# Kernel tuning notes

Measured on AMD Instinct MI355X. Metric: run time of the kernel, lower is better.

Reference implementation:

```python
import jax, jax.numpy as jnp
import numpy as np

N = 100000
E = 1600000
IN_C, HID, OUT_C = 3, 64, 1


def setup_inputs() -> dict:
    key = jax.random.key(0)
    ks = jax.random.split(key, 12)
    x = jax.random.normal(ks[0], (N, IN_C), dtype=jnp.float32)
    edge_index = jax.random.randint(ks[1], (2, E), 0, N, dtype=jnp.int64)

    def glorot(k, shape):
        lim = np.sqrt(6.0 / (shape[0] + shape[1]))
        return jax.random.uniform(k, shape, jnp.float32, -lim, lim)

    return {
        "x": x,
        "edge_index": edge_index,
        "W1": glorot(ks[2], (IN_C, HID)), "b1": jnp.zeros((HID,), jnp.float32),
        "W2": glorot(ks[3], (HID, HID)), "b2": jnp.zeros((HID,), jnp.float32),
        "W3": glorot(ks[4], (HID, HID)), "b3": jnp.zeros((HID,), jnp.float32),
        "Wm1": glorot(ks[5], (HID, HID)), "bm1": jnp.zeros((HID,), jnp.float32),
        "Wm2": glorot(ks[6], (HID, OUT_C)), "bm2": jnp.zeros((OUT_C,), jnp.float32),
    }


def gcn_conv(x, src, dst, W, b):
    """PyG GCNConv: symmetric normalization with self-loops, linear, scatter-add, bias."""
    n = x.shape[0]
    loop = jnp.arange(n, dtype=src.dtype)
    s = jnp.concatenate([src, loop])
    d = jnp.concatenate([dst, loop])
    h = x @ W  # (N, out)
    deg = jax.ops.segment_sum(jnp.ones(s.shape[0], dtype=h.dtype), d, num_segments=n)
    dinv = jnp.where(deg > 0, 1.0 / jnp.sqrt(jnp.where(deg > 0, deg, 1.0)), 0.0)
    norm = dinv[s] * dinv[d]  # (E+N,)
    out = jax.ops.segment_sum(h[s] * norm[:, None], d, num_segments=n)
    return out + b


def reference(x, edge_index, W1, b1, W2, b2, W3, b3, Wm1, bm1, Wm2, bm2):
    src, dst = edge_index[0], edge_index[1]
    # 3 GCN layers with ReLU (dropout inactive in eval mode)
    h = jax.nn.relu(gcn_conv(x, src, dst, W1, b1))
    h = jax.nn.relu(gcn_conv(h, src, dst, W2, b2))
    h = jax.nn.relu(gcn_conv(h, src, dst, W3, b3))
    # MLP head + sigmoid
    h = jax.nn.relu(h @ Wm1 + bm1)
    out = jax.nn.sigmoid(h @ Wm2 + bm2)  # (N, 1)
    return out
```

## Files before the change

### kernel.cpp

```cpp
#include <hip/hip_runtime.h>
#include <hip/hip_fp16.h>
#include <math.h>

#define N_NODES 100000
#define N_EDGES 1600000
#define EP (N_EDGES + N_NODES)
#define HID 64
#define NCHUNK 250
#define CE (N_EDGES / NCHUNK)
#define NBUCK 782
#define CAP 2816
#define NTILE (N_NODES / 16)
#define NPN 4

typedef _Float16 half8_t __attribute__((ext_vector_type(8)));
typedef _Float16 half4_t __attribute__((ext_vector_type(4)));
typedef float f32x4_t __attribute__((ext_vector_type(4)));
typedef unsigned long long u64;


__device__ __forceinline__ float fp8_to_f32_1(unsigned b) {
    unsigned s = b >> 7, e = (b >> 3) & 15, m = b & 7;
    float mag = (e == 0) ? (float)m * 0.001953125f
                         : __uint_as_float(((e + 120u) << 23) | (m << 20));
    return s ? -mag : mag;
}

__device__ __forceinline__ unsigned f32_to_fp8_1(float f) {
    unsigned sb = (__float_as_uint(f) >> 31) << 7;
    float a = fabsf(f);
    if (a > 448.f) a = 448.f;
    if (a < 0.001953125f * 0.5f) return sb;
    if (a < 0.015625f) {
        int q = (int)(a * 512.f + 0.5f);
        if (q > 7) return sb | (1u << 3);
        return sb | (unsigned)q;
    }
    unsigned bits = __float_as_uint(a) + (1u << 19);
    int e = (int)((bits >> 23) & 255) - 127;
    unsigned m = (bits >> 20) & 7;
    int ee = e + 7;
    if (ee > 15) { ee = 15; m = 6; }
    return sb | ((unsigned)ee << 3) | m;
}

__device__ __forceinline__ void addp8(float4& a, unsigned w, bool pred) {
    if (pred) {
#if __has_builtin(__builtin_amdgcn_cvt_pk_f32_fp8)
        auto lo = __builtin_amdgcn_cvt_pk_f32_fp8((int)w, false);
        auto hi = __builtin_amdgcn_cvt_pk_f32_fp8((int)w, true);
        a.x += lo[0]; a.y += lo[1]; a.z += hi[0]; a.w += hi[1];
#else
        a.x += fp8_to_f32_1(w & 255);
        a.y += fp8_to_f32_1((w >> 8) & 255);
        a.z += fp8_to_f32_1((w >> 16) & 255);
        a.w += fp8_to_f32_1(w >> 24);
#endif
    }
}

__device__ __forceinline__ unsigned pack_fp8x4(float a, float b, float c, float d) {
#if __has_builtin(__builtin_amdgcn_cvt_pk_fp8_f32)
    int v = 0;
    v = __builtin_amdgcn_cvt_pk_fp8_f32(a, b, v, false);
    v = __builtin_amdgcn_cvt_pk_fp8_f32(c, d, v, true);
    return (unsigned)v;
#else
    return f32_to_fp8_1(a) | (f32_to_fp8_1(b) << 8) |
           (f32_to_fp8_1(c) << 16) | (f32_to_fp8_1(d) << 24);
#endif
}


__global__ void init_kernel(int* __restrict__ gcur, int* __restrict__ csr) {
    int t = threadIdx.x;
    for (int b = t; b < NBUCK; b += 512) gcur[b] = b * CAP;
    if (t < 64) csr[EP + t] = 0;
}

__global__ __launch_bounds__(1024)
void scatter_kernel(const int* __restrict__ src, const int* __restrict__ dst,
                    int* __restrict__ gcur, unsigned* __restrict__ ebuf) {
    __shared__ int hist[NBUCK];
    __shared__ int cur[NBUCK];
    const int tid = threadIdx.x, c = blockIdx.x;
    for (int b = tid; b < NBUCK; b += 1024) hist[b] = 0;
    __syncthreads();
    const int4* d4p = (const int4*)(dst + c * CE);
    const int4* s4p = (const int4*)(src + c * CE);
    for (int t = tid; t < CE / 4; t += 1024) {
        int4 d = d4p[t];
        atomicAdd(&hist[d.x >> 7], 1);
        atomicAdd(&hist[d.y >> 7], 1);
        atomicAdd(&hist[d.z >> 7], 1);
        atomicAdd(&hist[d.w >> 7], 1);
    }
    __syncthreads();
    for (int b = tid; b < NBUCK; b += 1024)
        cur[b] = hist[b] ? atomicAdd(&gcur[b], hist[b]) : 0;
    __syncthreads();
    for (int t = tid; t < CE / 4; t += 1024) {
        int4 s = s4p[t];
        int4 d = d4p[t];
        int p0 = atomicAdd(&cur[d.x >> 7], 1);
        ebuf[p0] = ((unsigned)(d.x & 127) << 17) | (unsigned)s.x;
        int p1 = atomicAdd(&cur[d.y >> 7], 1);
        ebuf[p1] = ((unsigned)(d.y & 127) << 17) | (unsigned)s.y;
        int p2 = atomicAdd(&cur[d.z >> 7], 1);
        ebuf[p2] = ((unsigned)(d.z & 127) << 17) | (unsigned)s.z;
        int p3 = atomicAdd(&cur[d.w >> 7], 1);
        ebuf[p3] = ((unsigned)(d.w & 127) << 17) | (unsigned)s.w;
    }
}

__global__ __launch_bounds__(256)
void rankfill_kernel(const unsigned* __restrict__ ebuf, const int* __restrict__ gcur,
                     int* __restrict__ rowptr, int* __restrict__ csr,
                     float* __restrict__ dinv,
                     const float* __restrict__ x, float4* __restrict__ xd) {
    __shared__ unsigned stash[CAP];
    __shared__ int out[CAP + 128];
    __shared__ int cnt[128];
    __shared__ int cnt2[128];
    __shared__ int rpl8[128];
    __shared__ int wsum[2];
    __shared__ int sR0;
    const int tid = threadIdx.x, b = blockIdx.x;
    if (tid < 128) { cnt[tid] = 0; cnt2[tid] = 0; }
    if (tid == 0) sR0 = 0;
    __syncthreads();

    int acc = 0;
    for (int i = tid; i < b; i += 256) acc += gcur[i] - i * CAP + 128;
    if (acc) atomicAdd(&sR0, acc);

    const int E0 = b * CAP;
    const int RL = gcur[b] - E0;
    for (int off = tid; off < RL; off += 256) {
        unsigned v = ebuf[E0 + off];
        stash[off] = v;
        atomicAdd(&cnt[(v >> 17) & 0x7F], 1);
    }
    __syncthreads();
    const int R0 = sR0;

    const int lane = tid & 63, w = tid >> 6;
    int xcnt = (tid < 128) ? cnt[tid] : 0;
    int inc = xcnt;
#pragma unroll
    for (int off = 1; off < 64; off <<= 1) {
        int y = __shfl_up(inc, off, 64);
        if (lane >= off) inc += y;
    }
    if (lane == 63 && w < 2) wsum[w] = inc;
    __syncthreads();
    if (tid < 128) {
        int base = (w == 1) ? wsum[0] : 0;
        int rel = tid + base + inc - xcnt;
        rpl8[tid] = rel;
        const int n = b * 128 + tid;
        if (n < N_NODES) {
            rowptr[n] = R0 + rel;
            float di = rsqrtf((float)(xcnt + 1));
            dinv[n] = di;
            out[rel + xcnt] = n;
            xd[n] = make_float4(x[n * 3 + 0] * di, x[n * 3 + 1] * di, x[n * 3 + 2] * di, 0.f);
        }
    }
    if (b == NBUCK - 1 && tid == 0) rowptr[N_NODES] = EP;
    __syncthreads();

    for (int off = tid; off < RL; off += 256) {
        unsigned v = stash[off];
        int key = (v >> 17) & 0x7F;
        int r = atomicAdd(&cnt2[key], 1);
        out[rpl8[key] + r] = (int)(v & 0x1FFFFu);
    }
    __syncthreads();

    const int nreal = min(128, N_NODES - b * 128);
    const int lim = RL + nreal;
    for (int i = tid; i < lim; i += 256) csr[R0 + i] = out[i];
}


__device__ __forceinline__ void bfly_store_lds(float4 acc, const float4 b4, float di,
                                               int g, int p, int l, _Float16* __restrict__ tl) {
    acc.x += __shfl_xor(acc.x, 16, 64);
    acc.y += __shfl_xor(acc.y, 16, 64);
    acc.z += __shfl_xor(acc.z, 16, 64);
    acc.w += __shfl_xor(acc.w, 16, 64);
    acc.x += __shfl_xor(acc.x, 32, 64);
    acc.y += __shfl_xor(acc.y, 32, 64);
    acc.z += __shfl_xor(acc.z, 32, 64);
    acc.w += __shfl_xor(acc.w, 32, 64);
    if (g == 0) {
        half4_t hv;
        hv[0] = (_Float16)fmaxf(fmaf(di, acc.x, b4.x), 0.f);
        hv[1] = (_Float16)fmaxf(fmaf(di, acc.y, b4.y), 0.f);
        hv[2] = (_Float16)fmaxf(fmaf(di, acc.z, b4.z), 0.f);
        hv[3] = (_Float16)fmaxf(fmaf(di, acc.w, b4.w), 0.f);
        *(half4_t*)(tl + l * 72 + p * 4) = hv;
    }
}

__device__ __forceinline__ void gather_phase(const unsigned* __restrict__ gfq,
                                             const int* __restrict__ rowptr,
                                             const int* __restrict__ csr,
                                             const float* __restrict__ dinv,
                                             const float* __restrict__ bias,
                                             int n0, int lane, int wid,
                                             _Float16* __restrict__ tl) {
    const int g = lane >> 4, p = lane & 15;
    const int nw = n0 + wid * NPN;
    int rp = rowptr[nw + min(lane, NPN)];
    const float4 b4 = ((const float4*)bias)[p];
    int begv[NPN], cntv[NPN], idxv[NPN];
    int end_prev = __shfl(rp, 0, 64);
#pragma unroll
    for (int i = 0; i < NPN; ++i) {
        int end = __shfl(rp, i + 1, 64);
        begv[i] = end_prev;
        cntv[i] = end - end_prev;
        end_prev = end;
        idxv[i] = (lane < cntv[i]) ? csr[begv[i] + lane] : 0;
    }
#pragma unroll
    for (int ii = 0; ii < NPN; ii += 2) {
        const int la = wid * NPN + ii, lb = la + 1;
        const int ca = cntv[ii], cb = cntv[ii + 1];
        const int ba = begv[ii], bb = begv[ii + 1];
        const int iva = idxv[ii], ivb = idxv[ii + 1];
        int sa0 = __shfl(iva, g, 64),      sb0 = __shfl(ivb, g, 64);
        int sa1 = __shfl(iva, g + 4, 64),  sb1 = __shfl(ivb, g + 4, 64);
        int sa2 = __shfl(iva, g + 8, 64),  sb2 = __shfl(ivb, g + 8, 64);
        int sa3 = __shfl(iva, g + 12, 64), sb3 = __shfl(ivb, g + 12, 64);
        unsigned ua0 = gfq[(size_t)sa0 * 16 + p], ub0 = gfq[(size_t)sb0 * 16 + p];
        unsigned ua1 = gfq[(size_t)sa1 * 16 + p], ub1 = gfq[(size_t)sb1 * 16 + p];
        unsigned ua2 = gfq[(size_t)sa2 * 16 + p], ub2 = gfq[(size_t)sb2 * 16 + p];
        unsigned ua3 = gfq[(size_t)sa3 * 16 + p], ub3 = gfq[(size_t)sb3 * 16 + p];
        float4 accA = make_float4(0.f, 0.f, 0.f, 0.f);
        float4 accB = make_float4(0.f, 0.f, 0.f, 0.f);
        addp8(accA, ua0, g + 0 < ca);  addp8(accB, ub0, g + 0 < cb);
        addp8(accA, ua1, g + 4 < ca);  addp8(accB, ub1, g + 4 < cb);
        addp8(accA, ua2, g + 8 < ca);  addp8(accB, ub2, g + 8 < cb);
        addp8(accA, ua3, g + 12 < ca); addp8(accB, ub3, g + 12 < cb);
        if (ca > 16) {
#pragma unroll
            for (int k = 4; k < 8; ++k) {
                int e = g + 4 * k;
                int s = __shfl(iva, e, 64);
                addp8(accA, gfq[(size_t)s * 16 + p], e < ca);
            }
            if (ca > 32) {
                for (int e = 32 + g; e < ca; e += 4) {
                    int s = (e < 64) ? __shfl(iva, e, 64) : csr[ba + e];
                    addp8(accA, gfq[(size_t)s * 16 + p], true);
                }
            }
        }
        if (cb > 16) {
#pragma unroll
            for (int k = 4; k < 8; ++k) {
                int e = g + 4 * k;
                int s = __shfl(ivb, e, 64);
                addp8(accB, gfq[(size_t)s * 16 + p], e < cb);
            }
            if (cb > 32) {
                for (int e = 32 + g; e < cb; e += 4) {
                    int s = (e < 64) ? __shfl(ivb, e, 64) : csr[bb + e];
                    addp8(accB, gfq[(size_t)s * 16 + p], true);
                }
            }
        }
        bfly_store_lds(accA, b4, dinv[n0 + la], g, p, la, tl);
        bfly_store_lds(accB, b4, dinv[n0 + lb], g, p, lb, tl);
    }
}

__device__ __forceinline__ void mfma_fp8_store(const float* __restrict__ W,
                                               const float* __restrict__ dinv, int n0,
                                               int lane, int wid, int tid,
                                               _Float16* __restrict__ tile,
                                               _Float16* __restrict__ tile2,
                                               unsigned* __restrict__ gf_out) {
    const int kg = lane >> 4, n = lane & 15;
    half8_t B0, B1;
#pragma unroll
    for (int j = 0; j < 8; ++j) {
        B0[j] = (_Float16)W[(kg * 8 + j) * HID + wid * 16 + n];
        B1[j] = (_Float16)W[(32 + kg * 8 + j) * HID + wid * 16 + n];
    }
    half8_t A0 = *(const half8_t*)(tile + n * 72 + kg * 8);
    half8_t A1 = *(const half8_t*)(tile + n * 72 + 32 + kg * 8);
    f32x4_t c = {0.f, 0.f, 0.f, 0.f};
    c = __builtin_amdgcn_mfma_f32_16x16x32_f16(A0, B0, c, 0, 0, 0);
    c = __builtin_amdgcn_mfma_f32_16x16x32_f16(A1, B1, c, 0, 0, 0);
    const int q = lane >> 4;
#pragma unroll
    for (int r = 0; r < 4; ++r)
        tile2[(q * 4 + r) * 72 + wid * 16 + n] = (_Float16)(c[r] * dinv[n0 + q * 4 + r]);
    __syncthreads();
    const int row = tid >> 4, seg = tid & 15;
    uint2 v = *(const uint2*)(tile2 + row * 72 + seg * 4);
    __half2 h0 = *(__half2*)&v.x, h1 = *(__half2*)&v.y;
    float2 f0 = __half22float2(h0), f1 = __half22float2(h1);
    gf_out[(size_t)(n0 + row) * 16 + seg] = pack_fp8x4(f0.x, f0.y, f1.x, f1.y);
}


__global__ __launch_bounds__(256, 8)
void fused_layer1_kernel(const float4* __restrict__ xd, const int* __restrict__ rowptr,
                         const int* __restrict__ csr, const float* __restrict__ dinv,
                         const float* __restrict__ b1, const float* __restrict__ W1,
                         const float* __restrict__ W2, unsigned* __restrict__ gf_out) {
    __shared__ __align__(16) _Float16 tile[16 * 72];
    __shared__ __align__(16) _Float16 tile2[16 * 72];
    const int tid = threadIdx.x;
    const int lane = tid & 63, wid = tid >> 6;
    const int n0 = blockIdx.x * 16;

    const int j = lane >> 4, p0 = lane & 15;
    const int l = wid * 4 + j;
    const int node = n0 + l;
    const int beg = rowptr[node], end = rowptr[node + 1];
    float a0 = 0.f, a1 = 0.f, a2 = 0.f;
    for (int e = beg + p0; e < end; e += 16) {
        float4 v = xd[csr[e]];
        a0 += v.x; a1 += v.y; a2 += v.z;
    }
#pragma unroll
    for (int off = 1; off < 16; off <<= 1) {
        a0 += __shfl_xor(a0, off, 64);
        a1 += __shfl_xor(a1, off, 64);
        a2 += __shfl_xor(a2, off, 64);
    }
    const float dd = dinv[node];
    const float4 w0 = ((const float4*)W1)[p0];
    const float4 w1 = ((const float4*)(W1 + HID))[p0];
    const float4 w2 = ((const float4*)(W1 + 2 * HID))[p0];
    const float4 bb = ((const float4*)b1)[p0];
    half4_t hv;
    hv[0] = (_Float16)fmaxf(fmaf(dd, a0 * w0.x + a1 * w1.x + a2 * w2.x, bb.x), 0.f);
    hv[1] = (_Float16)fmaxf(fmaf(dd, a0 * w0.y + a1 * w1.y + a2 * w2.y, bb.y), 0.f);
    hv[2] = (_Float16)fmaxf(fmaf(dd, a0 * w0.z + a1 * w1.z + a2 * w2.z, bb.z), 0.f);
    hv[3] = (_Float16)fmaxf(fmaf(dd, a0 * w0.w + a1 * w1.w + a2 * w2.w, bb.w), 0.f);
    *(half4_t*)(tile + l * 72 + p0 * 4) = hv;
    __syncthreads();

    mfma_fp8_store(W2, dinv, n0, lane, wid, tid, tile, tile2, gf_out);
}

__global__ __launch_bounds__(256, 8)
void fused_layer_kernel(const unsigned* __restrict__ gf_in, const int* __restrict__ rowptr,
                        const int* __restrict__ csr, const float* __restrict__ dinv,
                        const float* __restrict__ bias, const float* __restrict__ W,
                        unsigned* __restrict__ gf_out) {
    __shared__ __align__(16) _Float16 tile[16 * 72];
    __shared__ __align__(16) _Float16 tile2[16 * 72];
    const int tid = threadIdx.x;
    const int lane = tid & 63, wid = tid >> 6;
    const int n0 = blockIdx.x * 16;

    gather_phase(gf_in, rowptr, csr, dinv, bias, n0, lane, wid, tile);
    __syncthreads();

    mfma_fp8_store(W, dinv, n0, lane, wid, tid, tile, tile2, gf_out);
}


__global__ __launch_bounds__(256, 8)
void fused_final_kernel(const unsigned* __restrict__ gf_in, const int* __restrict__ rowptr,
                        const int* __restrict__ csr, const float* __restrict__ dinv,
                        const float* __restrict__ b3, const float* __restrict__ Wm1,
                        const float* __restrict__ bm1, const float* __restrict__ Wm2,
                        const float* __restrict__ bm2, float* __restrict__ out) {
    __shared__ __align__(16) _Float16 tile[16 * 72];
    __shared__ float redbuf[4][16];
    const int tid = threadIdx.x;
    const int lane = tid & 63, wid = tid >> 6;
    const int n0 = blockIdx.x * 16;

    gather_phase(gf_in, rowptr, csr, dinv, b3, n0, lane, wid, tile);
    __syncthreads();

    const int kg = lane >> 4, n = lane & 15;
    half8_t B0, B1;
#pragma unroll
    for (int j = 0; j < 8; ++j) {
        B0[j] = (_Float16)Wm1[(kg * 8 + j) * HID + wid * 16 + n];
        B1[j] = (_Float16)Wm1[(32 + kg * 8 + j) * HID + wid * 16 + n];
    }
    half8_t A0 = *(const half8_t*)(tile + n * 72 + kg * 8);
    half8_t A1 = *(const half8_t*)(tile + n * 72 + 32 + kg * 8);
    f32x4_t c = {0.f, 0.f, 0.f, 0.f};
    c = __builtin_amdgcn_mfma_f32_16x16x32_f16(A0, B0, c, 0, 0, 0);
    c = __builtin_amdgcn_mfma_f32_16x16x32_f16(A1, B1, c, 0, 0, 0);

    const float bm1c = bm1[wid * 16 + n];
    const float wm2c = Wm2[wid * 16 + n];
    float part[4];
#pragma unroll
    for (int r = 0; r < 4; ++r) part[r] = fmaxf(c[r] + bm1c, 0.0f) * wm2c;
#pragma unroll
    for (int off = 1; off < 16; off <<= 1)
#pragma unroll
        for (int r = 0; r < 4; ++r) part[r] += __shfl_xor(part[r], off, 64);
    const int q = lane >> 4;
    if (n == 0) {
#pragma unroll
        for (int r = 0; r < 4; ++r) redbuf[wid][q * 4 + r] = part[r];
    }
    __syncthreads();
    if (tid < 16) {
        float s = redbuf[0][tid] + redbuf[1][tid] + redbuf[2][tid] + redbuf[3][tid];
        out[n0 + tid] = 1.0f / (1.0f + expf(-(s + bm2[0])));
    }
}


extern "C" void kernel_launch(void* const* d_in, const int* in_sizes, int n_in,
                              void* d_out, int out_size, void* d_ws, size_t ws_size,
                              hipStream_t stream) {
    const float* x   = (const float*)d_in[0];
    const int*   ei  = (const int*)d_in[1];
    const float* W1  = (const float*)d_in[2];
    const float* b1  = (const float*)d_in[3];
    const float* W2  = (const float*)d_in[4];
    const float* b2  = (const float*)d_in[5];
    const float* W3  = (const float*)d_in[6];
    const float* b3  = (const float*)d_in[7];
    const float* Wm1 = (const float*)d_in[8];
    const float* bm1 = (const float*)d_in[9];
    const float* Wm2 = (const float*)d_in[10];
    const float* bm2 = (const float*)d_in[11];
    float* out = (float*)d_out;

    const int* src = ei;
    const int* dst = ei + N_EDGES;

    char* ws = (char*)d_ws;
    size_t off = 0;
    auto alloc = [&](size_t bytes) { size_t o = off; off = (off + bytes + 255) & ~(size_t)255; return (void*)(ws + o); };
    int*      rowptr = (int*)alloc(4ll * (N_NODES + 1));
    int*      gcur   = (int*)alloc(4ll * NBUCK);
    int*      csr    = (int*)alloc(4ll * (EP + 64));
    float*    dinv   = (float*)alloc(4ll * N_NODES);
    float4*   xd     = (float4*)alloc(16ll * N_NODES);
    unsigned* gfA    = (unsigned*)alloc(4ll * N_NODES * 16);
    unsigned* gfB    = (unsigned*)alloc(4ll * N_NODES * 16);
    unsigned* ebuf   = (unsigned*)alloc(4ll * (size_t)NBUCK * CAP);
    (void)ws_size;

    init_kernel<<<1, 512, 0, stream>>>(gcur, csr);
    scatter_kernel<<<NCHUNK, 1024, 0, stream>>>(src, dst, gcur, ebuf);
    rankfill_kernel<<<NBUCK, 256, 0, stream>>>(ebuf, gcur, rowptr, csr, dinv, x, xd);

    fused_layer1_kernel<<<NTILE, 256, 0, stream>>>(xd, rowptr, csr, dinv, b1, W1, W2, gfB);
    fused_layer_kernel<<<NTILE, 256, 0, stream>>>(gfB, rowptr, csr, dinv, b2, W3, gfA);
    fused_final_kernel<<<NTILE, 256, 0, stream>>>(gfA, rowptr, csr, dinv, b3, Wm1, bm1, Wm2, bm2, out);
}
```

Baseline: 191.4 us.

## Replace LDS-histogram scatter with direct padded global atomics; load CSR indices directly in gather

The scatter kernel drops its per-chunk shared-memory histogram, prefix reservation and two-pass scheme. Each thread now atomically bumps a global per-bucket cursor, padded to one per 64-byte line to avoid false sharing. This removes one pass over the dst array and the block-level syncs, at the cost of 1.6M contended global atomics on only 782 counters. Separately, the gather phase stops preloading neighbor indices into lanes and shuffling them, and reads csr directly per group, trading shuffles for more (mostly cached) global loads.

```diff
diff --git a/kernel.cpp b/kernel.cpp
--- a/kernel.cpp
+++ b/kernel.cpp
@@ -6,12 +6,11 @@
 #define N_EDGES 1600000
 #define EP (N_EDGES + N_NODES)
 #define HID 64
-#define NCHUNK 250
-#define CE (N_EDGES / NCHUNK)
 #define NBUCK 782
 #define CAP 2816
 #define NTILE (N_NODES / 16)
 #define NPN 4
+#define SC_THREADS (N_EDGES / 4)
 
 typedef _Float16 half8_t __attribute__((ext_vector_type(8)));
 typedef _Float16 half4_t __attribute__((ext_vector_type(4)));
@@ -74,43 +73,25 @@
 
 __global__ void init_kernel(int* __restrict__ gcur, int* __restrict__ csr) {
     int t = threadIdx.x;
-    for (int b = t; b < NBUCK; b += 512) gcur[b] = b * CAP;
+    for (int b = t; b < NBUCK; b += 512) gcur[b * 16] = b * CAP;
     if (t < 64) csr[EP + t] = 0;
 }
 
 __global__ __launch_bounds__(1024)
 void scatter_kernel(const int* __restrict__ src, const int* __restrict__ dst,
                     int* __restrict__ gcur, unsigned* __restrict__ ebuf) {
-    __shared__ int hist[NBUCK];
-    __shared__ int cur[NBUCK];
-    const int tid = threadIdx.x, c = blockIdx.x;
-    for (int b = tid; b < NBUCK; b += 1024) hist[b] = 0;
-    __syncthreads();
-    const int4* d4p = (const int4*)(dst + c * CE);
-    const int4* s4p = (const int4*)(src + c * CE);
-    for (int t = tid; t < CE / 4; t += 1024) {
-        int4 d = d4p[t];
-        atomicAdd(&hist[d.x >> 7], 1);
-        atomicAdd(&hist[d.y >> 7], 1);
-        atomicAdd(&hist[d.z >> 7], 1);
-        atomicAdd(&hist[d.w >> 7], 1);
-    }
-    __syncthreads();
-    for (int b = tid; b < NBUCK; b += 1024)
-        cur[b] = hist[b] ? atomicAdd(&gcur[b], hist[b]) : 0;
-    __syncthreads();
-    for (int t = tid; t < CE / 4; t += 1024) {
-        int4 s = s4p[t];
-        int4 d = d4p[t];
-        int p0 = atomicAdd(&cur[d.x >> 7], 1);
-        ebuf[p0] = ((unsigned)(d.x & 127) << 17) | (unsigned)s.x;
-        int p1 = atomicAdd(&cur[d.y >> 7], 1);
-        ebuf[p1] = ((unsigned)(d.y & 127) << 17) | (unsigned)s.y;
-        int p2 = atomicAdd(&cur[d.z >> 7], 1);
-        ebuf[p2] = ((unsigned)(d.z & 127) << 17) | (unsigned)s.z;
-        int p3 = atomicAdd(&cur[d.w >> 7], 1);
-        ebuf[p3] = ((unsigned)(d.w & 127) << 17) | (unsigned)s.w;
-    }
+    int t = blockIdx.x * 1024 + threadIdx.x;
+    if (t >= SC_THREADS) return;
+    int4 d = ((const int4*)dst)[t];
+    int4 s = ((const int4*)src)[t];
+    int p0 = atomicAdd(&gcur[(d.x >> 7) * 16], 1);
+    ebuf[p0] = ((unsigned)(d.x & 127) << 17) | (unsigned)s.x;
+    int p1 = atomicAdd(&gcur[(d.y >> 7) * 16], 1);
+    ebuf[p1] = ((unsigned)(d.y & 127) << 17) | (unsigned)s.y;
+    int p2 = atomicAdd(&gcur[(d.z >> 7) * 16], 1);
+    ebuf[p2] = ((unsigned)(d.z & 127) << 17) | (unsigned)s.z;
+    int p3 = atomicAdd(&gcur[(d.w >> 7) * 16], 1);
+    ebuf[p3] = ((unsigned)(d.w & 127) << 17) | (unsigned)s.w;
 }
 
 __global__ __launch_bounds__(256)
@@ -131,11 +112,11 @@
     __syncthreads();
 
     int acc = 0;
-    for (int i = tid; i < b; i += 256) acc += gcur[i] - i * CAP + 128;
+    for (int i = tid; i < b; i += 256) acc += gcur[i * 16] - i * CAP + 128;
     if (acc) atomicAdd(&sR0, acc);
 
     const int E0 = b * CAP;
-    const int RL = gcur[b] - E0;
+    const int RL = gcur[b * 16] - E0;
     for (int off = tid; off < RL; off += 256) {
         unsigned v = ebuf[E0 + off];
         stash[off] = v;
@@ -215,7 +196,7 @@
     const int nw = n0 + wid * NPN;
     int rp = rowptr[nw + min(lane, NPN)];
     const float4 b4 = ((const float4*)bias)[p];
-    int begv[NPN], cntv[NPN], idxv[NPN];
+    int begv[NPN], cntv[NPN];
     int end_prev = __shfl(rp, 0, 64);
 #pragma unroll
     for (int i = 0; i < NPN; ++i) {
@@ -223,18 +204,20 @@
         begv[i] = end_prev;
         cntv[i] = end - end_prev;
         end_prev = end;
-        idxv[i] = (lane < cntv[i]) ? csr[begv[i] + lane] : 0;
     }
 #pragma unroll
     for (int ii = 0; ii < NPN; ii += 2) {
         const int la = wid * NPN + ii, lb = la + 1;
         const int ca = cntv[ii], cb = cntv[ii + 1];
         const int ba = begv[ii], bb = begv[ii + 1];
-        const int iva = idxv[ii], ivb = idxv[ii + 1];
-        int sa0 = __shfl(iva, g, 64),      sb0 = __shfl(ivb, g, 64);
-        int sa1 = __shfl(iva, g + 4, 64),  sb1 = __shfl(ivb, g + 4, 64);
-        int sa2 = __shfl(iva, g + 8, 64),  sb2 = __shfl(ivb, g + 8, 64);
-        int sa3 = __shfl(iva, g + 12, 64), sb3 = __shfl(ivb, g + 12, 64);
+        int sa0 = (g      < ca) ? csr[ba + g]      : 0;
+        int sb0 = (g      < cb) ? csr[bb + g]      : 0;
+        int sa1 = (g + 4  < ca) ? csr[ba + g + 4]  : 0;
+        int sb1 = (g + 4  < cb) ? csr[bb + g + 4]  : 0;
+        int sa2 = (g + 8  < ca) ? csr[ba + g + 8]  : 0;
+        int sb2 = (g + 8  < cb) ? csr[bb + g + 8]  : 0;
+        int sa3 = (g + 12 < ca) ? csr[ba + g + 12] : 0;
+        int sb3 = (g + 12 < cb) ? csr[bb + g + 12] : 0;
         unsigned ua0 = gfq[(size_t)sa0 * 16 + p], ub0 = gfq[(size_t)sb0 * 16 + p];
         unsigned ua1 = gfq[(size_t)sa1 * 16 + p], ub1 = gfq[(size_t)sb1 * 16 + p];
         unsigned ua2 = gfq[(size_t)sa2 * 16 + p], ub2 = gfq[(size_t)sb2 * 16 + p];
@@ -249,28 +232,24 @@
 #pragma unroll
             for (int k = 4; k < 8; ++k) {
                 int e = g + 4 * k;
-                int s = __shfl(iva, e, 64);
+                int s = (e < ca) ? csr[ba + e] : 0;
                 addp8(accA, gfq[(size_t)s * 16 + p], e < ca);
             }
             if (ca > 32) {
-                for (int e = 32 + g; e < ca; e += 4) {
-                    int s = (e < 64) ? __shfl(iva, e, 64) : csr[ba + e];
-                    addp8(accA, gfq[(size_t)s * 16 + p], true);
-                }
+                for (int e = 32 + g; e < ca; e += 4)
+                    addp8(accA, gfq[(size_t)csr[ba + e] * 16 + p], true);
             }
         }
         if (cb > 16) {
 #pragma unroll
             for (int k = 4; k < 8; ++k) {
                 int e = g + 4 * k;
-                int s = __shfl(ivb, e, 64);
+                int s = (e < cb) ? csr[bb + e] : 0;
                 addp8(accB, gfq[(size_t)s * 16 + p], e < cb);
             }
             if (cb > 32) {
-                for (int e = 32 + g; e < cb; e += 4) {
-                    int s = (e < 64) ? __shfl(ivb, e, 64) : csr[bb + e];
-                    addp8(accB, gfq[(size_t)s * 16 + p], true);
-                }
+                for (int e = 32 + g; e < cb; e += 4)
+                    addp8(accB, gfq[(size_t)csr[bb + e] * 16 + p], true);
             }
         }
         bfly_store_lds(accA, b4, dinv[n0 + la], g, p, la, tl);
@@ -443,7 +422,7 @@
     size_t off = 0;
     auto alloc = [&](size_t bytes) { size_t o = off; off = (off + bytes + 255) & ~(size_t)255; return (void*)(ws + o); };
     int*      rowptr = (int*)alloc(4ll * (N_NODES + 1));
-    int*      gcur   = (int*)alloc(4ll * NBUCK);
+    int*      gcur   = (int*)alloc(4ll * NBUCK * 16);
     int*      csr    = (int*)alloc(4ll * (EP + 64));
     float*    dinv   = (float*)alloc(4ll * N_NODES);
     float4*   xd     = (float4*)alloc(16ll * N_NODES);
@@ -453,7 +432,7 @@
     (void)ws_size;
 
     init_kernel<<<1, 512, 0, stream>>>(gcur, csr);
-    scatter_kernel<<<NCHUNK, 1024, 0, stream>>>(src, dst, gcur, ebuf);
+    scatter_kernel<<<(SC_THREADS + 1023) / 1024, 1024, 0, stream>>>(src, dst, gcur, ebuf);
     rankfill_kernel<<<NBUCK, 256, 0, stream>>>(ebuf, gcur, rowptr, csr, dinv, x, xd);
 
     fused_layer1_kernel<<<NTILE, 256, 0, stream>>>(xd, rowptr, csr, dinv, b1, W1, W2, gfB);
```

After: 287.2 us. 1.5x slower.
